# Performance work log

Hardware: AMD Instinct MI355X
Metric: run time of the kernel (lower is better)

The kernel has to match this reference:

```python
import jax, jax.numpy as jnp
import numpy as np

D_MODEL = 512
D_ATTN = 512

def setup_inputs() -> dict:
    key = jax.random.key(0)
    kx, kq, kk, kv = jax.random.split(key, 4)
    x = jax.random.normal(kx, (8, 2048, D_MODEL), dtype=jnp.float32)
    s = 1.0 / np.sqrt(D_MODEL)
    Wq = jax.random.normal(kq, (D_ATTN, D_MODEL), dtype=jnp.float32) * s
    Wk = jax.random.normal(kk, (D_ATTN, D_MODEL), dtype=jnp.float32) * s
    Wv = jax.random.normal(kv, (D_MODEL, D_MODEL), dtype=jnp.float32) * s
    return {"x": x, "Wq": Wq, "Wk": Wk, "Wv": Wv}

def reference(x, Wq, Wk, Wv):
    # x: [B, S, D]; Linear(bias=False): y = x @ W.T
    q = jnp.einsum('bsd,ad->bsa', x, Wq)  # [B,S,Da]
    k = jnp.einsum('bsd,ad->bsa', x, Wk)  # [B,S,Da]
    v = jnp.einsum('bsd,ed->bse', x, Wv)  # [B,S,Dv]
    scale = 1.0 / jnp.sqrt(jnp.asarray(q.shape[-1], dtype=q.dtype))
    scores = jnp.einsum('bqa,bka->bqk', q, k) * scale  # [B,S,S]
    p = jax.nn.softmax(scores, axis=-1)
    return jnp.einsum('bqk,bke->bqe', p, v)
```

## Files before the change

kernel.cpp:

```cpp
#include <hip/hip_runtime.h>


typedef __bf16 bf16x8 __attribute__((ext_vector_type(8)));
typedef __bf16 bf16x4 __attribute__((ext_vector_type(4)));
typedef float  f32x4  __attribute__((ext_vector_type(4)));

constexpr int SEQ = 2048;
constexpr int DM  = 512;
constexpr int NB  = 8;
constexpr int GS  = NB * SEQ;

__device__ __forceinline__ void gl16(const void* g, void* l) {
  __builtin_amdgcn_global_load_lds((const __attribute__((address_space(1))) void*)g,
                                   (__attribute__((address_space(3))) void*)l, 16, 0, 0);
}

__device__ __forceinline__ f32x4 mfma16(bf16x8 a, bf16x8 b, f32x4 c) {
  return __builtin_amdgcn_mfma_f32_16x16x32_bf16(a, b, c, 0, 0, 0);
}

__global__ void convert_kernel(const float* __restrict__ x,
                               const float* __restrict__ wq,
                               const float* __restrict__ wk,
                               const float* __restrict__ wv,
                               __bf16* __restrict__ xb,
                               __bf16* __restrict__ wqb,
                               __bf16* __restrict__ wkb,
                               __bf16* __restrict__ wvb) {
  const int NX4 = (GS * DM) / 4;
  const int NW4 = (DM * DM) / 4;
  const int stride = gridDim.x * blockDim.x;
  const int tid = blockIdx.x * blockDim.x + threadIdx.x;
  for (int i = tid; i < NX4; i += stride) {
    float4 v = ((const float4*)x)[i];
    bf16x4 o = { (__bf16)v.x, (__bf16)v.y, (__bf16)v.z, (__bf16)v.w };
    ((bf16x4*)xb)[i] = o;
  }
  for (int i = tid; i < NW4; i += stride) {
    float4 v = ((const float4*)wq)[i];
    bf16x4 o = { (__bf16)v.x, (__bf16)v.y, (__bf16)v.z, (__bf16)v.w };
    ((bf16x4*)wqb)[i] = o;
  }
  for (int i = tid; i < NW4; i += stride) {
    float4 v = ((const float4*)wk)[i];
    bf16x4 o = { (__bf16)v.x, (__bf16)v.y, (__bf16)v.z, (__bf16)v.w };
    ((bf16x4*)wkb)[i] = o;
  }
  for (int i = tid; i < NW4; i += stride) {
    float4 v = ((const float4*)wv)[i];
    bf16x4 o = { (__bf16)v.x, (__bf16)v.y, (__bf16)v.z, (__bf16)v.w };
    ((bf16x4*)wvb)[i] = o;
  }
}

__global__ __launch_bounds__(256, 2) void gemm_nt_kernel(
    const __bf16* __restrict__ A, const __bf16* __restrict__ Bm,
    __bf16* __restrict__ C, int N) {
  __shared__ __bf16 As[128 * 32];
  __shared__ __bf16 Bs[128 * 32];
  const int t = threadIdx.x;
  const int w = t >> 6, l = t & 63;
  const int l15 = l & 15, lg = l >> 4;
  const int m0 = blockIdx.x * 128, n0 = blockIdx.y * 128;
  const int wr = w >> 1, wc = w & 1;

  f32x4 acc[4][4] = {};
  const char* Ab = (const char*)A + (size_t)m0 * (DM * 2);
  const char* Bb = (const char*)Bm + (size_t)n0 * (DM * 2);

  for (int k0 = 0; k0 < DM; k0 += 32) {
#pragma unroll
    for (int i = 0; i < 2; ++i) {
      const int f = (i * 256 + t) * 16;
      const int row = f >> 6, c = f & 63;
      gl16(Ab + (size_t)row * (DM * 2) + k0 * 2 + c, (char*)As + f);
      gl16(Bb + (size_t)row * (DM * 2) + k0 * 2 + c, (char*)Bs + f);
    }
    __syncthreads();
    bf16x8 af[4], bfr[4];
#pragma unroll
    for (int mi = 0; mi < 4; ++mi)
      af[mi] = *(const bf16x8*)((const char*)As + (wr * 64 + mi * 16 + l15) * 64 + lg * 16);
#pragma unroll
    for (int ni = 0; ni < 4; ++ni)
      bfr[ni] = *(const bf16x8*)((const char*)Bs + (wc * 64 + ni * 16 + l15) * 64 + lg * 16);
#pragma unroll
    for (int mi = 0; mi < 4; ++mi)
#pragma unroll
      for (int ni = 0; ni < 4; ++ni)
        acc[mi][ni] = mfma16(af[mi], bfr[ni], acc[mi][ni]);
    __syncthreads();
  }
#pragma unroll
  for (int mi = 0; mi < 4; ++mi)
#pragma unroll
    for (int ni = 0; ni < 4; ++ni)
#pragma unroll
      for (int r = 0; r < 4; ++r) {
        const int row = m0 + wr * 64 + mi * 16 + lg * 4 + r;
        const int col = n0 + wc * 64 + ni * 16 + l15;
        C[(size_t)row * N + col] = (__bf16)acc[mi][ni][r];
      }
}

constexpr int NT = SEQ / 64;

__global__ __launch_bounds__(512, 2) void attn_kernel(
    const __bf16* __restrict__ Qg, const __bf16* __restrict__ Kg,
    const __bf16* __restrict__ Vt, float* __restrict__ Out) {
  __shared__ __bf16 Ks[64 * 512];
  __shared__ __bf16 Vs[512 * 64];
  __shared__ float  Ss[64 * 68];
  __shared__ __bf16 Ps[64 * 72];
  __shared__ float  m_s[64], l_s[64], corr_s[64];
  __shared__ int    flags_s[8];

  const int t = threadIdx.x;
  const int w = t >> 6, l = t & 63;
  const int l15 = l & 15, lg = l >> 4;
  const int b = blockIdx.y;
  const int q0 = blockIdx.x * 64;
  const int qi2 = w >> 2, kvq = w & 3;

  bf16x8 qf[2][16];
  {
    const char* Qb = (const char*)Qg +
        ((size_t)(b * SEQ + q0 + qi2 * 32 + l15) * DM) * 2 + lg * 16;
#pragma unroll
    for (int mi = 0; mi < 2; ++mi)
#pragma unroll
      for (int ks = 0; ks < 16; ++ks)
        qf[mi][ks] = *(const bf16x8*)(Qb + (size_t)mi * 16 * DM * 2 + ks * 64);
  }

  f32x4 o[4][4] = {};

  if (t < 64) { m_s[t] = -__builtin_inff(); l_s[t] = 0.f; }

  const char* Kb = (const char*)Kg + (size_t)b * SEQ * DM * 2;
  const char* Vb = (const char*)Vt + (size_t)b * SEQ * 2;

#pragma unroll
  for (int i = 0; i < 8; ++i) {
    const int f = (i * 512 + t) * 16;
    const int row = f >> 10, c = f & 1023;
    const int sc = c ^ ((row & 7) << 4);
    gl16(Kb + (size_t)row * 1024 + sc, (char*)Ks + f);
  }
  __syncthreads();

  const float SCL = 0.0637639022f;

  for (int it = 0; it < NT; ++it) {
    const int kv0 = it * 64;

#pragma unroll
    for (int i = 0; i < 8; ++i) {
      const int f = (i * 512 + t) * 16;
      const int e = f >> 7, c2 = f & 127;
      const int sc2 = c2 ^ ((e & 7) << 4);
      gl16(Vb + (size_t)e * (GS * 2) + (size_t)kv0 * 2 + sc2, (char*)Vs + f);
    }
    {
      f32x4 sa0 = {}, sa1 = {};
      const int krow = kvq * 16 + l15;
      const char* KsR = (const char*)Ks + krow * 1024;
      const int ksw = (krow & 7) << 4;
#pragma unroll
      for (int ks = 0; ks < 16; ++ks) {
        bf16x8 kf = *(const bf16x8*)(KsR + ((ks * 64 + lg * 16) ^ ksw));
        sa0 = mfma16(qf[0][ks], kf, sa0);
        sa1 = mfma16(qf[1][ks], kf, sa1);
      }
#pragma unroll
      for (int r = 0; r < 4; ++r) {
        Ss[(qi2 * 32 + lg * 4 + r) * 68 + kvq * 16 + l15] = sa0[r] * SCL;
        Ss[(qi2 * 32 + 16 + lg * 4 + r) * 68 + kvq * 16 + l15] = sa1[r] * SCL;
      }
    }
    __syncthreads();

    {
      const int row = w * 8 + (l >> 3), c8 = l & 7;
      const float* Sr = &Ss[row * 68 + c8 * 8];
      float4 v0 = *(const float4*)(Sr);
      float4 v1 = *(const float4*)(Sr + 4);
      float tmax = fmaxf(fmaxf(fmaxf(v0.x, v0.y), fmaxf(v0.z, v0.w)),
                         fmaxf(fmaxf(v1.x, v1.y), fmaxf(v1.z, v1.w)));
      tmax = fmaxf(tmax, __shfl_xor(tmax, 1));
      tmax = fmaxf(tmax, __shfl_xor(tmax, 2));
      tmax = fmaxf(tmax, __shfl_xor(tmax, 4));
      const float mold = m_s[row];
      const float mnew = fmaxf(mold, tmax);
      const float corr = exp2f(mold - mnew);
      const float p0 = exp2f(v0.x - mnew), p1 = exp2f(v0.y - mnew);
      const float p2 = exp2f(v0.z - mnew), p3 = exp2f(v0.w - mnew);
      const float p4 = exp2f(v1.x - mnew), p5 = exp2f(v1.y - mnew);
      const float p6 = exp2f(v1.z - mnew), p7 = exp2f(v1.w - mnew);
      float rsum = ((p0 + p1) + (p2 + p3)) + ((p4 + p5) + (p6 + p7));
      rsum += __shfl_xor(rsum, 1);
      rsum += __shfl_xor(rsum, 2);
      rsum += __shfl_xor(rsum, 4);
      const float lnew = l_s[row] * corr + rsum;
      if (c8 == 0) { m_s[row] = mnew; l_s[row] = lnew; corr_s[row] = corr; }
      const int allskip = __all(corr == 1.0f);
      if (l == 0) flags_s[w] = allskip;
      bf16x8 pb = { (__bf16)p0, (__bf16)p1, (__bf16)p2, (__bf16)p3,
                    (__bf16)p4, (__bf16)p5, (__bf16)p6, (__bf16)p7 };
      *(bf16x8*)((char*)Ps + row * 144 + c8 * 16) = pb;
    }
    __syncthreads();

    {
      const int kvn = ((it + 1) == NT ? 0 : (it + 1)) * 64;
#pragma unroll
      for (int i = 0; i < 8; ++i) {
        const int f = (i * 512 + t) * 16;
        const int row = f >> 10, c = f & 1023;
        const int sc = c ^ ((row & 7) << 4);
        gl16(Kb + (size_t)(kvn + row) * 1024 + sc, (char*)Ks + f);
      }
      const int flag = flags_s[l & 7];
      if (!__all(flag != 0)) {
#pragma unroll
        for (int mi = 0; mi < 4; ++mi) {
          float cr[4];
#pragma unroll
          for (int r = 0; r < 4; ++r) cr[r] = corr_s[mi * 16 + lg * 4 + r];
#pragma unroll
          for (int ni = 0; ni < 4; ++ni)
#pragma unroll
            for (int r = 0; r < 4; ++r) o[mi][ni][r] *= cr[r];
        }
      }
#pragma unroll
      for (int ks = 0; ks < 2; ++ks) {
        bf16x8 pf[4];
#pragma unroll
        for (int mi = 0; mi < 4; ++mi)
          pf[mi] = *(const bf16x8*)((const char*)Ps + (mi * 16 + l15) * 144 + ks * 64 + lg * 16);
#pragma unroll
        for (int ni = 0; ni < 4; ++ni) {
          const int er = w * 64 + ni * 16 + l15;
          bf16x8 vf = *(const bf16x8*)((const char*)Vs + er * 128 +
                                       ((ks * 64 + lg * 16) ^ ((er & 7) << 4)));
#pragma unroll
          for (int mi = 0; mi < 4; ++mi)
            o[mi][ni] = mfma16(pf[mi], vf, o[mi][ni]);
        }
      }
    }
    __syncthreads();
  }

#pragma unroll
  for (int mi = 0; mi < 4; ++mi) {
    float rl[4];
#pragma unroll
    for (int r = 0; r < 4; ++r) rl[r] = 1.0f / l_s[mi * 16 + lg * 4 + r];
#pragma unroll
    for (int ni = 0; ni < 4; ++ni)
#pragma unroll
      for (int r = 0; r < 4; ++r) {
        const int row = q0 + mi * 16 + lg * 4 + r;
        const int col = w * 64 + ni * 16 + l15;
        Out[((size_t)b * SEQ + row) * DM + col] = o[mi][ni][r] * rl[r];
      }
  }
}

extern "C" void kernel_launch(void* const* d_in, const int* in_sizes, int n_in,
                              void* d_out, int out_size, void* d_ws, size_t ws_size,
                              hipStream_t stream) {
  const float* x  = (const float*)d_in[0];
  const float* wq = (const float*)d_in[1];
  const float* wk = (const float*)d_in[2];
  const float* wv = (const float*)d_in[3];
  float* out = (float*)d_out;
  char* ws = (char*)d_ws;

  __bf16* xb  = (__bf16*)(ws);
  __bf16* wqb = (__bf16*)(ws + 16777216);
  __bf16* wkb = (__bf16*)(ws + 17301504);
  __bf16* wvb = (__bf16*)(ws + 17825792);
  __bf16* Qg  = (__bf16*)(ws + 18350080);
  __bf16* Kg  = (__bf16*)(ws + 35127296);
  __bf16* Vt  = (__bf16*)(ws + 51904512);

  convert_kernel<<<2048, 256, 0, stream>>>(x, wq, wk, wv, xb, wqb, wkb, wvb);
  gemm_nt_kernel<<<dim3(GS / 128, DM / 128), 256, 0, stream>>>(xb, wqb, Qg, DM);
  gemm_nt_kernel<<<dim3(GS / 128, DM / 128), 256, 0, stream>>>(xb, wkb, Kg, DM);
  gemm_nt_kernel<<<dim3(DM / 128, GS / 128), 256, 0, stream>>>(wvb, xb, Vt, GS);
  attn_kernel<<<dim3(SEQ / 64, NB), 512, 0, stream>>>(Qg, Kg, Vt, out);
}
```

Baseline: 316.1 us.

## Fuse Q/K projections into one GEMM and shrink attention tiles to 32

```diff
diff --git a/kernel.cpp b/kernel.cpp
--- a/kernel.cpp
+++ b/kernel.cpp
@@ -9,6 +9,7 @@
 constexpr int DM  = 512;
 constexpr int NB  = 8;
 constexpr int GS  = NB * SEQ;
+constexpr int NT2 = SEQ / 32;
 
 __device__ __forceinline__ void gl16(const void* g, void* l) {
   __builtin_amdgcn_global_load_lds((const __attribute__((address_space(1))) void*)g,
@@ -103,90 +104,79 @@
       }
 }
 
-constexpr int NT = SEQ / 64;
-
-__global__ __launch_bounds__(512, 2) void attn_kernel(
-    const __bf16* __restrict__ Qg, const __bf16* __restrict__ Kg,
-    const __bf16* __restrict__ Vt, float* __restrict__ Out) {
-  __shared__ __bf16 Ks[64 * 512];
-  __shared__ __bf16 Vs[512 * 64];
-  __shared__ float  Ss[64 * 68];
-  __shared__ __bf16 Ps[64 * 72];
-  __shared__ float  m_s[64], l_s[64], corr_s[64];
-  __shared__ int    flags_s[8];
+__global__ __launch_bounds__(256, 2) void attn_kernel(
+    const __bf16* __restrict__ QK, const __bf16* __restrict__ Vt,
+    float* __restrict__ Out) {
+  __shared__ __bf16 Ks[32 * 512];
+  __shared__ __bf16 Vs[512 * 32];
+  __shared__ float  Ss[32 * 36];
+  __shared__ __bf16 Ps[32 * 32];
+  __shared__ float  m_s[32], l_s[32], corr_s[32];
+  __shared__ int    flags_s[4];
 
   const int t = threadIdx.x;
   const int w = t >> 6, l = t & 63;
   const int l15 = l & 15, lg = l >> 4;
-  const int b = blockIdx.y;
-  const int q0 = blockIdx.x * 64;
-  const int qi2 = w >> 2, kvq = w & 3;
-
-  bf16x8 qf[2][16];
+  const int bid = blockIdx.x;
+  const int b = bid & 7;
+  const int q0 = (bid >> 3) * 32;
+  const int qi = w >> 1, kj = w & 1;
+
+  bf16x8 qf[16];
   {
-    const char* Qb = (const char*)Qg +
-        ((size_t)(b * SEQ + q0 + qi2 * 32 + l15) * DM) * 2 + lg * 16;
-#pragma unroll
-    for (int mi = 0; mi < 2; ++mi)
-#pragma unroll
-      for (int ks = 0; ks < 16; ++ks)
-        qf[mi][ks] = *(const bf16x8*)(Qb + (size_t)mi * 16 * DM * 2 + ks * 64);
-  }
-
-  f32x4 o[4][4] = {};
-
-  if (t < 64) { m_s[t] = -__builtin_inff(); l_s[t] = 0.f; }
-
-  const char* Kb = (const char*)Kg + (size_t)b * SEQ * DM * 2;
+    const char* Qb = (const char*)QK +
+        (size_t)(b * SEQ + q0 + qi * 16 + l15) * 2048 + lg * 16;
+#pragma unroll
+    for (int ks = 0; ks < 16; ++ks)
+      qf[ks] = *(const bf16x8*)(Qb + ks * 64);
+  }
+
+  f32x4 o[2][8] = {};
+  if (t < 32) { m_s[t] = -__builtin_inff(); l_s[t] = 0.f; }
+
+  const char* Kb = (const char*)QK + (size_t)b * SEQ * 2048 + 1024;
   const char* Vb = (const char*)Vt + (size_t)b * SEQ * 2;
 
 #pragma unroll
   for (int i = 0; i < 8; ++i) {
-    const int f = (i * 512 + t) * 16;
+    const int f = (i * 256 + t) * 16;
     const int row = f >> 10, c = f & 1023;
-    const int sc = c ^ ((row & 7) << 4);
-    gl16(Kb + (size_t)row * 1024 + sc, (char*)Ks + f);
+    gl16(Kb + (size_t)row * 2048 + (c ^ ((row & 7) << 4)), (char*)Ks + f);
   }
   __syncthreads();
 
   const float SCL = 0.0637639022f;
 
-  for (int it = 0; it < NT; ++it) {
-    const int kv0 = it * 64;
+  for (int it = 0; it < NT2; ++it) {
+    const int kv0 = it * 32;
 
 #pragma unroll
     for (int i = 0; i < 8; ++i) {
-      const int f = (i * 512 + t) * 16;
-      const int e = f >> 7, c2 = f & 127;
-      const int sc2 = c2 ^ ((e & 7) << 4);
-      gl16(Vb + (size_t)e * (GS * 2) + (size_t)kv0 * 2 + sc2, (char*)Vs + f);
+      const int f = (i * 256 + t) * 16;
+      const int e = f >> 6, c2 = f & 63;
+      gl16(Vb + (size_t)e * (GS * 2) + (size_t)kv0 * 2 + (c2 ^ ((e & 3) << 4)),
+           (char*)Vs + f);
     }
     {
-      f32x4 sa0 = {}, sa1 = {};
-      const int krow = kvq * 16 + l15;
+      f32x4 sa = {};
+      const int krow = kj * 16 + l15;
       const char* KsR = (const char*)Ks + krow * 1024;
       const int ksw = (krow & 7) << 4;
 #pragma unroll
       for (int ks = 0; ks < 16; ++ks) {
         bf16x8 kf = *(const bf16x8*)(KsR + ((ks * 64 + lg * 16) ^ ksw));
-        sa0 = mfma16(qf[0][ks], kf, sa0);
-        sa1 = mfma16(qf[1][ks], kf, sa1);
-      }
-#pragma unroll
-      for (int r = 0; r < 4; ++r) {
-        Ss[(qi2 * 32 + lg * 4 + r) * 68 + kvq * 16 + l15] = sa0[r] * SCL;
-        Ss[(qi2 * 32 + 16 + lg * 4 + r) * 68 + kvq * 16 + l15] = sa1[r] * SCL;
-      }
+        sa = mfma16(qf[ks], kf, sa);
+      }
+#pragma unroll
+      for (int r = 0; r < 4; ++r)
+        Ss[(qi * 16 + lg * 4 + r) * 36 + kj * 16 + l15] = sa[r] * SCL;
     }
     __syncthreads();
 
     {
-      const int row = w * 8 + (l >> 3), c8 = l & 7;
-      const float* Sr = &Ss[row * 68 + c8 * 8];
-      float4 v0 = *(const float4*)(Sr);
-      float4 v1 = *(const float4*)(Sr + 4);
-      float tmax = fmaxf(fmaxf(fmaxf(v0.x, v0.y), fmaxf(v0.z, v0.w)),
-                         fmaxf(fmaxf(v1.x, v1.y), fmaxf(v1.z, v1.w)));
+      const int row = t >> 3, c8 = t & 7;
+      float4 v0 = *(const float4*)&Ss[row * 36 + c8 * 4];
+      float tmax = fmaxf(fmaxf(v0.x, v0.y), fmaxf(v0.z, v0.w));
       tmax = fmaxf(tmax, __shfl_xor(tmax, 1));
       tmax = fmaxf(tmax, __shfl_xor(tmax, 2));
       tmax = fmaxf(tmax, __shfl_xor(tmax, 4));
@@ -195,75 +185,71 @@
       const float corr = exp2f(mold - mnew);
       const float p0 = exp2f(v0.x - mnew), p1 = exp2f(v0.y - mnew);
       const float p2 = exp2f(v0.z - mnew), p3 = exp2f(v0.w - mnew);
-      const float p4 = exp2f(v1.x - mnew), p5 = exp2f(v1.y - mnew);
-      const float p6 = exp2f(v1.z - mnew), p7 = exp2f(v1.w - mnew);
-      float rsum = ((p0 + p1) + (p2 + p3)) + ((p4 + p5) + (p6 + p7));
+      float rsum = (p0 + p1) + (p2 + p3);
       rsum += __shfl_xor(rsum, 1);
       rsum += __shfl_xor(rsum, 2);
       rsum += __shfl_xor(rsum, 4);
-      const float lnew = l_s[row] * corr + rsum;
-      if (c8 == 0) { m_s[row] = mnew; l_s[row] = lnew; corr_s[row] = corr; }
+      if (c8 == 0) { m_s[row] = mnew; l_s[row] = l_s[row] * corr + rsum; corr_s[row] = corr; }
       const int allskip = __all(corr == 1.0f);
       if (l == 0) flags_s[w] = allskip;
-      bf16x8 pb = { (__bf16)p0, (__bf16)p1, (__bf16)p2, (__bf16)p3,
-                    (__bf16)p4, (__bf16)p5, (__bf16)p6, (__bf16)p7 };
-      *(bf16x8*)((char*)Ps + row * 144 + c8 * 16) = pb;
+      bf16x4 pb = { (__bf16)p0, (__bf16)p1, (__bf16)p2, (__bf16)p3 };
+      *(bf16x4*)((char*)Ps + row * 64 + (((c8 >> 1) * 16) ^ ((row & 3) << 4)) +
+                 (c8 & 1) * 8) = pb;
     }
     __syncthreads();
 
     {
-      const int kvn = ((it + 1) == NT ? 0 : (it + 1)) * 64;
+      const int kvn = ((it + 1) == NT2 ? 0 : (it + 1)) * 32;
 #pragma unroll
       for (int i = 0; i < 8; ++i) {
-        const int f = (i * 512 + t) * 16;
+        const int f = (i * 256 + t) * 16;
         const int row = f >> 10, c = f & 1023;
-        const int sc = c ^ ((row & 7) << 4);
-        gl16(Kb + (size_t)(kvn + row) * 1024 + sc, (char*)Ks + f);
-      }
-      const int flag = flags_s[l & 7];
-      if (!__all(flag != 0)) {
-#pragma unroll
-        for (int mi = 0; mi < 4; ++mi) {
+        gl16(Kb + (size_t)(kvn + row) * 2048 + (c ^ ((row & 7) << 4)), (char*)Ks + f);
+      }
+      const int fl = flags_s[0] & flags_s[1] & flags_s[2] & flags_s[3];
+      if (!fl) {
+#pragma unroll
+        for (int mi = 0; mi < 2; ++mi) {
           float cr[4];
 #pragma unroll
           for (int r = 0; r < 4; ++r) cr[r] = corr_s[mi * 16 + lg * 4 + r];
 #pragma unroll
-          for (int ni = 0; ni < 4; ++ni)
+          for (int ni = 0; ni < 8; ++ni)
 #pragma unroll
             for (int r = 0; r < 4; ++r) o[mi][ni][r] *= cr[r];
         }
       }
-#pragma unroll
-      for (int ks = 0; ks < 2; ++ks) {
-        bf16x8 pf[4];
-#pragma unroll
-        for (int mi = 0; mi < 4; ++mi)
-          pf[mi] = *(const bf16x8*)((const char*)Ps + (mi * 16 + l15) * 144 + ks * 64 + lg * 16);
-#pragma unroll
-        for (int ni = 0; ni < 4; ++ni) {
-          const int er = w * 64 + ni * 16 + l15;
-          bf16x8 vf = *(const bf16x8*)((const char*)Vs + er * 128 +
-                                       ((ks * 64 + lg * 16) ^ ((er & 7) << 4)));
-#pragma unroll
-          for (int mi = 0; mi < 4; ++mi)
-            o[mi][ni] = mfma16(pf[mi], vf, o[mi][ni]);
-        }
-      }
-    }
-    __syncthreads();
-  }
-
-#pragma unroll
-  for (int mi = 0; mi < 4; ++mi) {
+      bf16x8 pf[2];
+#pragma unroll
+      for (int mi = 0; mi < 2; ++mi) {
+        const int prow = mi * 16 + l15;
+        pf[mi] = *(const bf16x8*)((const char*)Ps + prow * 64 +
+                                  ((lg * 16) ^ ((prow & 3) << 4)));
+      }
+#pragma unroll
+      for (int ni = 0; ni < 8; ++ni) {
+        const int er = w * 128 + ni * 16 + l15;
+        bf16x8 vf = *(const bf16x8*)((const char*)Vs + er * 64 +
+                                     ((lg * 16) ^ ((er & 3) << 4)));
+#pragma unroll
+        for (int mi = 0; mi < 2; ++mi)
+          o[mi][ni] = mfma16(pf[mi], vf, o[mi][ni]);
+      }
+    }
+    __syncthreads();
+  }
+
+#pragma unroll
+  for (int mi = 0; mi < 2; ++mi) {
     float rl[4];
 #pragma unroll
     for (int r = 0; r < 4; ++r) rl[r] = 1.0f / l_s[mi * 16 + lg * 4 + r];
 #pragma unroll
-    for (int ni = 0; ni < 4; ++ni)
+    for (int ni = 0; ni < 8; ++ni)
 #pragma unroll
       for (int r = 0; r < 4; ++r) {
         const int row = q0 + mi * 16 + lg * 4 + r;
-        const int col = w * 64 + ni * 16 + l15;
+        const int col = w * 128 + ni * 16 + l15;
         Out[((size_t)b * SEQ + row) * DM + col] = o[mi][ni][r] * rl[r];
       }
   }
@@ -279,17 +265,15 @@
   float* out = (float*)d_out;
   char* ws = (char*)d_ws;
 
-  __bf16* xb  = (__bf16*)(ws);
-  __bf16* wqb = (__bf16*)(ws + 16777216);
-  __bf16* wkb = (__bf16*)(ws + 17301504);
-  __bf16* wvb = (__bf16*)(ws + 17825792);
-  __bf16* Qg  = (__bf16*)(ws + 18350080);
-  __bf16* Kg  = (__bf16*)(ws + 35127296);
-  __bf16* Vt  = (__bf16*)(ws + 51904512);
-
-  convert_kernel<<<2048, 256, 0, stream>>>(x, wq, wk, wv, xb, wqb, wkb, wvb);
-  gemm_nt_kernel<<<dim3(GS / 128, DM / 128), 256, 0, stream>>>(xb, wqb, Qg, DM);
-  gemm_nt_kernel<<<dim3(GS / 128, DM / 128), 256, 0, stream>>>(xb, wkb, Kg, DM);
-  gemm_nt_kernel<<<dim3(DM / 128, GS / 128), 256, 0, stream>>>(wvb, xb, Vt, GS);
-  attn_kernel<<<dim3(SEQ / 64, NB), 512, 0, stream>>>(Qg, Kg, Vt, out);
-}
+  __bf16* xb   = (__bf16*)(ws);
+  __bf16* wqkb = (__bf16*)(ws + 16777216);
+  __bf16* wvb  = (__bf16*)(ws + 17825792);
+  __bf16* qk   = (__bf16*)(ws + 18350080);
+  __bf16* vt   = (__bf16*)(ws + 51904512);
+
+  convert_kernel<<<2048, 256, 0, stream>>>(x, wq, wk, wv,
+                                           xb, wqkb, wqkb + 262144, wvb);
+  gemm_nt_kernel<<<dim3(GS / 128, 1024 / 128), 256, 0, stream>>>(xb, wqkb, qk, 1024);
+  gemm_nt_kernel<<<dim3(DM / 128, GS / 128), 256, 0, stream>>>(wvb, xb, vt, GS);
+  attn_kernel<<<512, 256, 0, stream>>>(qk, vt, out);
+}
```

After: 273.3 us. -13.5%, faster.
